# Optimization experiments

Hardware: AMD Instinct MI355X
Metric: run time of the kernel (lower is better)

## Reference

```python
import jax, jax.numpy as jnp
import numpy as np

BN_EPS = 1e-5


def setup_inputs() -> dict:
    key = jax.random.key(0)
    ks = jax.random.split(key, 10)
    N, E, D = 100000, 1600000, 64
    node_feats = jax.random.normal(ks[0], (N, D), dtype=jnp.float32)
    edge_feats = jax.random.randint(ks[1], (E, 3), 0, 2, dtype=jnp.int64)
    edge_index = jax.random.randint(ks[2], (2, E), 0, N, dtype=jnp.int64)
    return {
        "node_feats": node_feats,
        "edge_feats": edge_feats,
        "edge_index": edge_index,
        "num_nodes": N,
        "num_edges": E,
        "eps": jnp.zeros((1,), jnp.float32),
        "bond_emb0": jax.random.normal(ks[3], (5, D), dtype=jnp.float32) * 0.05,
        "bond_emb1": jax.random.normal(ks[4], (6, D), dtype=jnp.float32) * 0.05,
        "bond_emb2": jax.random.normal(ks[5], (2, D), dtype=jnp.float32) * 0.05,
        "W1": jax.random.normal(ks[6], (2 * D, D), dtype=jnp.float32) * (1.0 / np.sqrt(D)),
        "b1": jnp.zeros((2 * D,), jnp.float32),
        "gamma": jnp.ones((2 * D,), jnp.float32),
        "beta": jnp.zeros((2 * D,), jnp.float32),
        "W2": jax.random.normal(ks[7], (D, 2 * D), dtype=jnp.float32) * (1.0 / np.sqrt(2 * D)),
        "b2": jnp.zeros((D,), jnp.float32),
    }


def reference(node_feats, edge_feats, edge_index, num_nodes, num_edges,
              eps, bond_emb0, bond_emb1, bond_emb2,
              W1, b1, gamma, beta, W2, b2):
    # BondEncoder: sum of categorical embeddings over 3 bond features -> [E, D]
    edge_emb = (bond_emb0[edge_feats[:, 0]]
                + bond_emb1[edge_feats[:, 1]]
                + bond_emb2[edge_feats[:, 2]])
    # gather source-node feats (edge_index[1]), combine, relu -> [E, D]
    message = jax.nn.relu(node_feats[edge_index[1]] + edge_emb)
    # scatter_add into target nodes (edge_index[0]) -> [N, D]
    message_reduce = jax.ops.segment_sum(message, edge_index[0], num_segments=num_nodes)
    h = (1.0 + eps) * node_feats + message_reduce  # eps shape [1] broadcasts
    # MLP: Linear -> BatchNorm1d (training-mode batch stats) -> ReLU -> Linear
    h1 = h @ W1.T + b1  # [N, 2D]
    mean = jnp.mean(h1, axis=0)
    var = jnp.mean(jnp.square(h1 - mean), axis=0)  # biased variance (torch BN)
    h1 = gamma * (h1 - mean) * jax.lax.rsqrt(var + BN_EPS) + beta
    h1 = jax.nn.relu(h1)
    return h1 @ W2.T + b2  # [N, D]
```

## Files before the change

### kernel.cpp

```cpp
#include <hip/hip_runtime.h>
#include <stdint.h>

#define D    64
#define D2   128
#define R    98
#define NBK  1024
#define CAP  2176
#define NTRI 2144

__global__ void k_embsum(
    const float* __restrict__ be0, const float* __restrict__ be1,
    const float* __restrict__ be2, float* __restrict__ embsum,
    int* __restrict__ bcursor)
{
    int c = blockIdx.x;
    int t = threadIdx.x;
    if (c < 60) {
        int f0 = c / 12;
        int r  = c % 12;
        int f1 = r / 2;
        int f2 = r % 2;
        embsum[c * D + t] = be0[f0 * D + t] + be1[f1 * D + t] + be2[f2 * D + t];
    } else {
        int i = (c - 60) * 64 + t;
        if (i < NBK) bcursor[i * 16] = i * CAP;
    }
}

__global__ __launch_bounds__(512) void k_part(
    const int* __restrict__ ei, const int* __restrict__ ef,
    int* __restrict__ bcursor, int* __restrict__ payload, int E)
{
    __shared__ int scnt[NBK];
    __shared__ int sstart[NBK];
    __shared__ int sgbase[NBK];
    __shared__ int sdat[4096];
    __shared__ unsigned short sbkt[4096];
    __shared__ int sred2[512];

    int t = threadIdx.x;
    for (int i = t; i < NBK; i += 512) scnt[i] = 0;
    __syncthreads();

    int base2 = blockIdx.x * 2048;

    int b0[4], p0[4], r0[4];
    int b1[4], p1[4], r1[4];

    #pragma unroll
    for (int k = 0; k < 4; k++) {
        int i2 = base2 + k * 512 + t;
        int e0 = i2 * 2;
        if (e0 < E) {
            int2 d  = ((const int2*)ei)[i2];
            int2 s  = ((const int2*)(ei + E))[i2];
            int2 q0 = ((const int2*)ef)[3 * i2 + 0];
            int2 q1 = ((const int2*)ef)[3 * i2 + 1];
            int2 q2 = ((const int2*)ef)[3 * i2 + 2];
            {
                int bb = d.x / R; if (bb > NBK - 1) bb = NBK - 1;
                int ld = d.x - bb * R;
                int code = q0.x * 12 + q0.y * 2 + q1.x;
                b0[k] = bb;
                p0[k] = s.x | (code << 17) | (ld << 23);
                r0[k] = atomicAdd(&scnt[bb], 1);
            }
            if (e0 + 1 < E) {
                int bb = d.y / R; if (bb > NBK - 1) bb = NBK - 1;
                int ld = d.y - bb * R;
                int code = q1.y * 12 + q2.x * 2 + q2.y;
                b1[k] = bb;
                p1[k] = s.y | (code << 17) | (ld << 23);
                r1[k] = atomicAdd(&scnt[bb], 1);
            }
        }
    }
    __syncthreads();

    int c0 = scnt[t * 2], c1 = scnt[t * 2 + 1];
    sred2[t] = c0 + c1;
    __syncthreads();
    int sv = sred2[t];
    for (int off = 1; off < 512; off <<= 1) {
        int x = (t >= off) ? sred2[t - off] : 0;
        __syncthreads();
        sred2[t] += x;
        __syncthreads();
    }
    int excl = sred2[t] - sv;
    sstart[t * 2]     = excl;
    sstart[t * 2 + 1] = excl + c0;
    __syncthreads();

    for (int i = t; i < NBK; i += 512) {
        int c = scnt[i];
        if (c) sgbase[i] = atomicAdd(&bcursor[i * 16], c);
    }
    __syncthreads();

    #pragma unroll
    for (int k = 0; k < 4; k++) {
        int i2 = base2 + k * 512 + t;
        int e0 = i2 * 2;
        if (e0 < E) {
            int slot = sstart[b0[k]] + r0[k];
            sdat[slot] = p0[k]; sbkt[slot] = (unsigned short)b0[k];
            if (e0 + 1 < E) {
                slot = sstart[b1[k]] + r1[k];
                sdat[slot] = p1[k]; sbkt[slot] = (unsigned short)b1[k];
            }
        }
    }
    __syncthreads();

    int tc = E - base2 * 2; if (tc > 4096) tc = 4096;
    #pragma unroll
    for (int k = 0; k < 8; k++) {
        int i = k * 512 + t;
        if (i < tc) {
            int bb = sbkt[i];
            int pos = sgbase[bb] + (i - sstart[bb]);
            if (pos < (bb + 1) * CAP) payload[pos] = sdat[i];
        }
    }
}

__global__ __launch_bounds__(512, 8) void k_sortred(
    const float* __restrict__ nf,
    const int* __restrict__ bcursor,
    int* __restrict__ payload,
    const float* __restrict__ embsum,
    const float* __restrict__ epsp,
    float* __restrict__ h, int N)
{
    __shared__ float sE[60 * D];
    __shared__ int   sq[CAP];
    __shared__ int   scn[R + 1];
    __shared__ int   scur[R];
    __shared__ int   sscan[128];

    int tid = threadIdx.x;
    int b = blockIdx.x;
    int n0 = b * R;

    for (int i = tid; i < 60 * D; i += 512) sE[i] = embsum[i];
    if (tid <= R) scn[tid] = 0;
    __syncthreads();

    int js = b * CAP;
    int cnt = bcursor[b * 16] - js;
    if (cnt > CAP) cnt = CAP;
    if (cnt < 0) cnt = 0;

    for (int i = tid; i < cnt; i += 512)
        atomicAdd(&scn[((unsigned)payload[js + i] >> 23) + 1], 1);
    __syncthreads();

    if (tid < 128) sscan[tid] = (tid <= R) ? scn[tid] : 0;
    __syncthreads();
    for (int off = 1; off < 128; off <<= 1) {
        int x = 0;
        if (tid < 128 && tid >= off) x = sscan[tid - off];
        __syncthreads();
        if (tid < 128) sscan[tid] += x;
        __syncthreads();
    }
    if (tid <= R) {
        scn[tid] = sscan[tid];
        if (tid < R) scur[tid] = sscan[tid];
    }
    __syncthreads();

    for (int i = tid; i < cnt; i += 512) {
        int u = payload[js + i];
        int pos = atomicAdd(&scur[(unsigned)u >> 23], 1);
        sq[pos] = u;
    }
    __syncthreads();

    int w = tid >> 6, l = tid & 63;
    float epsv = 1.0f + epsp[0];
    for (int r = w; r < R; r += 8) {
        int n = n0 + r;
        if (n >= N) break;
        int st = scn[r], en = scn[r + 1];
        float acc = 0.0f;
        for (int jb = st; jb < en; jb += 64) {
            int u = (jb + l < en) ? sq[jb + l] : 0;
            int m = en - jb; if (m > 64) m = 64;
            int t = 0;
            for (; t + 4 <= m; t += 4) {
                int a0 = __shfl(u, t + 0);
                int a1 = __shfl(u, t + 1);
                int a2 = __shfl(u, t + 2);
                int a3 = __shfl(u, t + 3);
                float x0 = nf[(size_t)(a0 & 0x1FFFF) * D + l];
                float x1 = nf[(size_t)(a1 & 0x1FFFF) * D + l];
                float x2 = nf[(size_t)(a2 & 0x1FFFF) * D + l];
                float x3 = nf[(size_t)(a3 & 0x1FFFF) * D + l];
                float e0 = sE[((a0 >> 17) & 63) * D + l];
                float e1 = sE[((a1 >> 17) & 63) * D + l];
                float e2 = sE[((a2 >> 17) & 63) * D + l];
                float e3 = sE[((a3 >> 17) & 63) * D + l];
                acc += fmaxf(x0 + e0, 0.0f) + fmaxf(x1 + e1, 0.0f)
                     + fmaxf(x2 + e2, 0.0f) + fmaxf(x3 + e3, 0.0f);
            }
            for (; t < m; t++) {
                int a = __shfl(u, t);
                acc += fmaxf(nf[(size_t)(a & 0x1FFFF) * D + l]
                             + sE[((a >> 17) & 63) * D + l], 0.0f);
            }
        }
        h[(size_t)n * D + l] = fmaf(epsv, nf[(size_t)n * D + l], acc);
    }
    __syncthreads();

    float* P = (float*)(payload + (size_t)b * CAP);
    const float4* h4 = (const float4*)h;
    if (tid < 256) {
        int iB = tid >> 4, jB = tid & 15;
        float M[4][4];
        #pragma unroll
        for (int a = 0; a < 4; a++)
            #pragma unroll
            for (int c = 0; c < 4; c++) M[a][c] = 0.0f;
        #pragma unroll 2
        for (int n2 = 0; n2 < R; n2++) {
            int n = n0 + n2;
            if (n >= N) break;
            float4 a = h4[(size_t)n * 16 + iB];
            float4 c = h4[(size_t)n * 16 + jB];
            M[0][0] = fmaf(a.x, c.x, M[0][0]);
            M[0][1] = fmaf(a.x, c.y, M[0][1]);
            M[0][2] = fmaf(a.x, c.z, M[0][2]);
            M[0][3] = fmaf(a.x, c.w, M[0][3]);
            M[1][0] = fmaf(a.y, c.x, M[1][0]);
            M[1][1] = fmaf(a.y, c.y, M[1][1]);
            M[1][2] = fmaf(a.y, c.z, M[1][2]);
            M[1][3] = fmaf(a.y, c.w, M[1][3]);
            M[2][0] = fmaf(a.z, c.x, M[2][0]);
            M[2][1] = fmaf(a.z, c.y, M[2][1]);
            M[2][2] = fmaf(a.z, c.z, M[2][2]);
            M[2][3] = fmaf(a.z, c.w, M[2][3]);
            M[3][0] = fmaf(a.w, c.x, M[3][0]);
            M[3][1] = fmaf(a.w, c.y, M[3][1]);
            M[3][2] = fmaf(a.w, c.z, M[3][2]);
            M[3][3] = fmaf(a.w, c.w, M[3][3]);
        }
        #pragma unroll
        for (int a = 0; a < 4; a++)
            #pragma unroll
            for (int c = 0; c < 4; c++) {
                int gi = iB * 4 + a, gj = jB * 4 + c;
                if (gi <= gj)
                    P[gi * 64 + gj - ((gi * (gi + 1)) >> 1)] = M[a][c];
            }
    } else if (tid < 320) {
        int lc = tid - 256;
        float s = 0.0f;
        for (int n2 = 0; n2 < R; n2++) {
            int n = n0 + n2;
            if (n >= N) break;
            s += h[(size_t)n * D + lc];
        }
        P[2080 + lc] = s;
    }
}

__global__ __launch_bounds__(512) void k_redM(
    const float* __restrict__ pM, int nblk,
    float* __restrict__ Mbar, float invN)
{
    __shared__ float sred[512];
    int tid = threadIdx.x;
    int eq = tid & 63, bq = tid >> 6;
    int e = blockIdx.x * 64 + eq;

    int src;
    if (e < 4096) {
        int i = e >> 6, j = e & 63;
        int a = i < j ? i : j;
        int b2 = i < j ? j : i;
        src = a * 64 + b2 - ((a * (a + 1)) >> 1);
    } else {
        src = 2080 + (e - 4096);
    }

    float s0 = 0.0f, s1 = 0.0f, s2 = 0.0f, s3 = 0.0f;
    int b = bq;
    for (; b + 24 < nblk; b += 32) {
        s0 += pM[(size_t)(b +  0) * CAP + src];
        s1 += pM[(size_t)(b +  8) * CAP + src];
        s2 += pM[(size_t)(b + 16) * CAP + src];
        s3 += pM[(size_t)(b + 24) * CAP + src];
    }
    for (; b < nblk; b += 8) s0 += pM[(size_t)b * CAP + src];
    sred[tid] = (s0 + s1) + (s2 + s3);
    __syncthreads();
    if (tid < 64) {
        float s = 0.0f;
        #pragma unroll
        for (int q = 0; q < 8; q++) s += sred[q * 64 + tid];
        Mbar[e] = s * invN;
    }
}

__global__ __launch_bounds__(64) void k_bn(
    const float* __restrict__ Mbar,
    const float* __restrict__ W1,
    const float* __restrict__ b1,
    const float* __restrict__ gamma, const float* __restrict__ beta,
    float* __restrict__ ss)
{
    int c = blockIdx.x;
    int k = threadIdx.x;

    float wk = W1[c * D + k];
    float dk = wk * Mbar[4096 + k];

    float tk = 0.0f;
    #pragma unroll 8
    for (int j = 0; j < 64; j++)
        tk = fmaf(Mbar[k * 64 + j], W1[c * D + j], tk);
    float qk = wk * tk;

    #pragma unroll
    for (int off = 32; off > 0; off >>= 1) {
        dk += __shfl_xor(dk, off);
        qk += __shfl_xor(qk, off);
    }

    if (k == 0) {
        float var  = fmaxf(qk - dk * dk, 0.0f);
        float mean = dk + b1[c];
        float sc   = gamma[c] * rsqrtf(var + 1e-5f);
        ss[c]       = sc;
        ss[128 + c] = beta[c] - mean * sc;
    }
}

#define ABS 132
__global__ __launch_bounds__(512) void k_gemm2(
    const float* __restrict__ h,
    const float* __restrict__ W1,
    const float* __restrict__ b1,
    const float* __restrict__ ss,
    const float* __restrict__ W2,
    const float* __restrict__ b2v,
    float* __restrict__ out,
    int N, int tiles)
{
    __shared__ float AB[128 * ABS];
    __shared__ float W1t[64 * 128];
    __shared__ float W2t[128 * 64];

    int tid = threadIdx.x;

    {
        int c  = tid >> 2;
        int k0 = (tid & 3) * 16;
        const float4* wr = (const float4*)(W1 + c * D + k0);
        #pragma unroll
        for (int q = 0; q < 4; q++) {
            float4 u = wr[q];
            int k = k0 + q * 4;
            W1t[(k + 0) * 128 + c] = u.x;
            W1t[(k + 1) * 128 + c] = u.y;
            W1t[(k + 2) * 128 + c] = u.z;
            W1t[(k + 3) * 128 + c] = u.w;
        }
    }
    {
        int j  = tid >> 3;
        int k0 = (tid & 7) * 16;
        const float4* wr = (const float4*)(W2 + j * D2 + k0);
        #pragma unroll
        for (int q = 0; q < 4; q++) {
            float4 u = wr[q];
            int k = k0 + q * 4;
            W2t[(k + 0) * 64 + j] = u.x;
            W2t[(k + 1) * 64 + j] = u.y;
            W2t[(k + 2) * 64 + j] = u.z;
            W2t[(k + 3) * 64 + j] = u.w;
        }
    }

    int rg = tid >> 5, cg = tid & 31;
    float bb0 = b1[cg * 4 + 0];
    float bb1 = b1[cg * 4 + 1];
    float bb2 = b1[cg * 4 + 2];
    float bb3 = b1[cg * 4 + 3];
    float4 scv = *(const float4*)&ss[cg * 4];
    float4 shv = *(const float4*)&ss[128 + cg * 4];

    int r2 = tid >> 4, c2 = tid & 15;
    float4 obv = *(const float4*)&b2v[c2 * 4];

    int sr = tid >> 2;
    int sc16 = (tid & 3) * 16;

    float4 pf[4];
    #pragma unroll
    for (int q = 0; q < 4; q++) pf[q] = make_float4(0.f, 0.f, 0.f, 0.f);
    {
        int gr = blockIdx.x * 128 + sr;
        if (gr < N) {
            const float4* hrow = (const float4*)(h + (size_t)gr * D + sc16);
            #pragma unroll
            for (int q = 0; q < 4; q++) pf[q] = hrow[q];
        }
    }

    for (int t = blockIdx.x; t < tiles; t += gridDim.x) {
        int row0 = t * 128;
        __syncthreads();
        {
            float* dstp = &AB[sr * ABS + sc16];
            #pragma unroll
            for (int q = 0; q < 4; q++) ((float4*)dstp)[q] = pf[q];
        }
        __syncthreads();

        float acc[8][4];
        #pragma unroll
        for (int i = 0; i < 8; i++)
            #pragma unroll
            for (int j = 0; j < 4; j++) acc[i][j] = 0.0f;

        #pragma unroll 2
        for (int k4 = 0; k4 < 16; k4++) {
            float4 w0 = *(const float4*)&W1t[(k4 * 4 + 0) * 128 + cg * 4];
            float4 w1 = *(const float4*)&W1t[(k4 * 4 + 1) * 128 + cg * 4];
            float4 w2 = *(const float4*)&W1t[(k4 * 4 + 2) * 128 + cg * 4];
            float4 w3 = *(const float4*)&W1t[(k4 * 4 + 3) * 128 + cg * 4];
            #pragma unroll
            for (int i = 0; i < 8; i++) {
                float4 a = *(const float4*)&AB[(rg * 8 + i) * ABS + k4 * 4];
                acc[i][0] = fmaf(a.x, w0.x, acc[i][0]);
                acc[i][1] = fmaf(a.x, w0.y, acc[i][1]);
                acc[i][2] = fmaf(a.x, w0.z, acc[i][2]);
                acc[i][3] = fmaf(a.x, w0.w, acc[i][3]);
                acc[i][0] = fmaf(a.y, w1.x, acc[i][0]);
                acc[i][1] = fmaf(a.y, w1.y, acc[i][1]);
                acc[i][2] = fmaf(a.y, w1.z, acc[i][2]);
                acc[i][3] = fmaf(a.y, w1.w, acc[i][3]);
                acc[i][0] = fmaf(a.z, w2.x, acc[i][0]);
                acc[i][1] = fmaf(a.z, w2.y, acc[i][1]);
                acc[i][2] = fmaf(a.z, w2.z, acc[i][2]);
                acc[i][3] = fmaf(a.z, w2.w, acc[i][3]);
                acc[i][0] = fmaf(a.w, w3.x, acc[i][0]);
                acc[i][1] = fmaf(a.w, w3.y, acc[i][1]);
                acc[i][2] = fmaf(a.w, w3.z, acc[i][2]);
                acc[i][3] = fmaf(a.w, w3.w, acc[i][3]);
            }
        }
        __syncthreads();

        int tn = t + gridDim.x;
        #pragma unroll
        for (int q = 0; q < 4; q++) pf[q] = make_float4(0.f, 0.f, 0.f, 0.f);
        if (tn < tiles) {
            int gr = tn * 128 + sr;
            if (gr < N) {
                const float4* hrow = (const float4*)(h + (size_t)gr * D + sc16);
                #pragma unroll
                for (int q = 0; q < 4; q++) pf[q] = hrow[q];
            }
        }

        #pragma unroll
        for (int i = 0; i < 8; i++) {
            float g0 = fmaxf(fmaf(acc[i][0] + bb0, scv.x, shv.x), 0.0f);
            float g1 = fmaxf(fmaf(acc[i][1] + bb1, scv.y, shv.y), 0.0f);
            float g2 = fmaxf(fmaf(acc[i][2] + bb2, scv.z, shv.z), 0.0f);
            float g3 = fmaxf(fmaf(acc[i][3] + bb3, scv.w, shv.w), 0.0f);
            *(float4*)&AB[(rg * 8 + i) * ABS + cg * 4] = make_float4(g0, g1, g2, g3);
        }
        __syncthreads();

        float acc2[4][4];
        #pragma unroll
        for (int i = 0; i < 4; i++)
            #pragma unroll
            for (int j = 0; j < 4; j++) acc2[i][j] = 0.0f;

        #pragma unroll 2
        for (int k4 = 0; k4 < 32; k4++) {
            float4 u0 = *(const float4*)&W2t[(k4 * 4 + 0) * 64 + c2 * 4];
            float4 u1 = *(const float4*)&W2t[(k4 * 4 + 1) * 64 + c2 * 4];
            float4 u2 = *(const float4*)&W2t[(k4 * 4 + 2) * 64 + c2 * 4];
            float4 u3 = *(const float4*)&W2t[(k4 * 4 + 3) * 64 + c2 * 4];
            #pragma unroll
            for (int i = 0; i < 4; i++) {
                float4 g = *(const float4*)&AB[(r2 * 4 + i) * ABS + k4 * 4];
                acc2[i][0] = fmaf(g.x, u0.x, acc2[i][0]);
                acc2[i][1] = fmaf(g.x, u0.y, acc2[i][1]);
                acc2[i][2] = fmaf(g.x, u0.z, acc2[i][2]);
                acc2[i][3] = fmaf(g.x, u0.w, acc2[i][3]);
                acc2[i][0] = fmaf(g.y, u1.x, acc2[i][0]);
                acc2[i][1] = fmaf(g.y, u1.y, acc2[i][1]);
                acc2[i][2] = fmaf(g.y, u1.z, acc2[i][2]);
                acc2[i][3] = fmaf(g.y, u1.w, acc2[i][3]);
                acc2[i][0] = fmaf(g.z, u2.x, acc2[i][0]);
                acc2[i][1] = fmaf(g.z, u2.y, acc2[i][1]);
                acc2[i][2] = fmaf(g.z, u2.z, acc2[i][2]);
                acc2[i][3] = fmaf(g.z, u2.w, acc2[i][3]);
                acc2[i][0] = fmaf(g.w, u3.x, acc2[i][0]);
                acc2[i][1] = fmaf(g.w, u3.y, acc2[i][1]);
                acc2[i][2] = fmaf(g.w, u3.z, acc2[i][2]);
                acc2[i][3] = fmaf(g.w, u3.w, acc2[i][3]);
            }
        }

        #pragma unroll
        for (int i = 0; i < 4; i++) {
            int gr = row0 + r2 * 4 + i;
            if (gr < N) {
                float4 pk = make_float4(acc2[i][0] + obv.x, acc2[i][1] + obv.y,
                                        acc2[i][2] + obv.z, acc2[i][3] + obv.w);
                *(float4*)&out[(size_t)gr * D + c2 * 4] = pk;
            }
        }
    }
}

extern "C" void kernel_launch(void* const* d_in, const int* in_sizes, int n_in,
                              void* d_out, int out_size, void* d_ws, size_t ws_size,
                              hipStream_t stream)
{
    const float* nf    = (const float*)d_in[0];
    const int*   ef    = (const int*)d_in[1];
    const int*   ei    = (const int*)d_in[2];
    const float* epsp  = (const float*)d_in[5];
    const float* be0   = (const float*)d_in[6];
    const float* be1   = (const float*)d_in[7];
    const float* be2   = (const float*)d_in[8];
    const float* W1    = (const float*)d_in[9];
    const float* b1    = (const float*)d_in[10];
    const float* gamma = (const float*)d_in[11];
    const float* beta  = (const float*)d_in[12];
    const float* W2    = (const float*)d_in[13];
    const float* b2v   = (const float*)d_in[14];
    float*       out   = (float*)d_out;

    int N = in_sizes[0] / D;
    int E = in_sizes[1] / 3;

    int tiles2 = (N + 127) / 128;
    int g2 = 256;

    float* h       = (float*)d_ws;
    float* Mbar    = h + (size_t)N * D;
    float* ss      = Mbar + 4224;
    float* embsum  = ss + 256;
    int*   bcursor = (int*)(embsum + 60 * D);
    int*   payload = bcursor + NBK * 16;
    float* pM      = (float*)payload;

    k_embsum<<<76, 64, 0, stream>>>(be0, be1, be2, embsum, bcursor);

    int E2 = (E + 1) / 2;
    int gP = (E2 + 2047) / 2048;
    k_part<<<gP, 512, 0, stream>>>(ei, ef, bcursor, payload, E);

    k_sortred<<<NBK, 512, 0, stream>>>(nf, bcursor, payload, embsum, epsp, h, N);

    k_redM<<<65, 512, 0, stream>>>(pM, NBK, Mbar, 1.0f / (float)N);
    k_bn<<<128, 64, 0, stream>>>(Mbar, W1, b1, gamma, beta, ss);

    k_gemm2<<<g2, 512, 0, stream>>>(h, W1, b1, ss, W2, b2v, out, N, tiles2);
}
```

Baseline: 351.3 us.

## Split sortred and gemm2 launches in halves and parallelize Mbar reduction with atomics

Splits k_sortred and k_gemm2 each into two half-size launches on the same stream. It also widens k_redM from 65 to 260 blocks, each summing a quarter of the partial blocks and combining results with atomicAdd into Mbar, which k_embsum now zeroes. The wider reduction targets poor occupancy in k_redM. The launch splitting adds launch overhead and gives no overlap on a single stream. The atomic accumulation also makes summation order nondeterministic.

```diff
diff --git a/kernel.cpp b/kernel.cpp
--- a/kernel.cpp
+++ b/kernel.cpp
@@ -11,7 +11,7 @@
 __global__ void k_embsum(
     const float* __restrict__ be0, const float* __restrict__ be1,
     const float* __restrict__ be2, float* __restrict__ embsum,
-    int* __restrict__ bcursor)
+    int* __restrict__ bcursor, float* __restrict__ Mbar)
 {
     int c = blockIdx.x;
     int t = threadIdx.x;
@@ -21,9 +21,12 @@
         int f1 = r / 2;
         int f2 = r % 2;
         embsum[c * D + t] = be0[f0 * D + t] + be1[f1 * D + t] + be2[f2 * D + t];
-    } else {
+    } else if (c < 76) {
         int i = (c - 60) * 64 + t;
         if (i < NBK) bcursor[i * 16] = i * CAP;
+    } else {
+        int i = (c - 76) * 64 + t;
+        Mbar[i] = 0.0f;
     }
 }
 
@@ -131,7 +134,7 @@
     int* __restrict__ payload,
     const float* __restrict__ embsum,
     const float* __restrict__ epsp,
-    float* __restrict__ h, int N)
+    float* __restrict__ h, int N, int b0)
 {
     __shared__ float sE[60 * D];
     __shared__ int   sq[CAP];
@@ -140,7 +143,7 @@
     __shared__ int   sscan[128];
 
     int tid = threadIdx.x;
-    int b = blockIdx.x;
+    int b = b0 + blockIdx.x;
     int n0 = b * R;
 
     for (int i = tid; i < 60 * D; i += 512) sE[i] = embsum[i];
@@ -268,13 +271,15 @@
 }
 
 __global__ __launch_bounds__(512) void k_redM(
-    const float* __restrict__ pM, int nblk,
+    const float* __restrict__ pM,
     float* __restrict__ Mbar, float invN)
 {
     __shared__ float sred[512];
     int tid = threadIdx.x;
     int eq = tid & 63, bq = tid >> 6;
-    int e = blockIdx.x * 64 + eq;
+    int ec = blockIdx.x >> 2;
+    int qg = blockIdx.x & 3;
+    int e  = ec * 64 + eq;
 
     int src;
     if (e < 4096) {
@@ -286,22 +291,21 @@
         src = 2080 + (e - 4096);
     }
 
+    int bbase = qg * 256;
     float s0 = 0.0f, s1 = 0.0f, s2 = 0.0f, s3 = 0.0f;
-    int b = bq;
-    for (; b + 24 < nblk; b += 32) {
-        s0 += pM[(size_t)(b +  0) * CAP + src];
-        s1 += pM[(size_t)(b +  8) * CAP + src];
-        s2 += pM[(size_t)(b + 16) * CAP + src];
-        s3 += pM[(size_t)(b + 24) * CAP + src];
-    }
-    for (; b < nblk; b += 8) s0 += pM[(size_t)b * CAP + src];
+    for (int b = bq; b < 256; b += 32) {
+        s0 += pM[(size_t)(bbase + b +  0) * CAP + src];
+        s1 += pM[(size_t)(bbase + b +  8) * CAP + src];
+        s2 += pM[(size_t)(bbase + b + 16) * CAP + src];
+        s3 += pM[(size_t)(bbase + b + 24) * CAP + src];
+    }
     sred[tid] = (s0 + s1) + (s2 + s3);
     __syncthreads();
     if (tid < 64) {
         float s = 0.0f;
         #pragma unroll
         for (int q = 0; q < 8; q++) s += sred[q * 64 + tid];
-        Mbar[e] = s * invN;
+        atomicAdd(&Mbar[e], s * invN);
     }
 }
 
@@ -348,7 +352,7 @@
     const float* __restrict__ W2,
     const float* __restrict__ b2v,
     float* __restrict__ out,
-    int N, int tiles)
+    int N, int tBeg, int tEnd)
 {
     __shared__ float AB[128 * ABS];
     __shared__ float W1t[64 * 128];
@@ -403,7 +407,7 @@
     #pragma unroll
     for (int q = 0; q < 4; q++) pf[q] = make_float4(0.f, 0.f, 0.f, 0.f);
     {
-        int gr = blockIdx.x * 128 + sr;
+        int gr = (tBeg + blockIdx.x) * 128 + sr;
         if (gr < N) {
             const float4* hrow = (const float4*)(h + (size_t)gr * D + sc16);
             #pragma unroll
@@ -411,7 +415,7 @@
         }
     }
 
-    for (int t = blockIdx.x; t < tiles; t += gridDim.x) {
+    for (int t = tBeg + blockIdx.x; t < tEnd; t += gridDim.x) {
         int row0 = t * 128;
         __syncthreads();
         {
@@ -459,7 +463,7 @@
         int tn = t + gridDim.x;
         #pragma unroll
         for (int q = 0; q < 4; q++) pf[q] = make_float4(0.f, 0.f, 0.f, 0.f);
-        if (tn < tiles) {
+        if (tn < tEnd) {
             int gr = tn * 128 + sr;
             if (gr < N) {
                 const float4* hrow = (const float4*)(h + (size_t)gr * D + sc16);
@@ -547,7 +551,7 @@
     int E = in_sizes[1] / 3;
 
     int tiles2 = (N + 127) / 128;
-    int g2 = 256;
+    int tMid   = (tiles2 + 1) / 2;
 
     float* h       = (float*)d_ws;
     float* Mbar    = h + (size_t)N * D;
@@ -557,16 +561,18 @@
     int*   payload = bcursor + NBK * 16;
     float* pM      = (float*)payload;
 
-    k_embsum<<<76, 64, 0, stream>>>(be0, be1, be2, embsum, bcursor);
+    k_embsum<<<142, 64, 0, stream>>>(be0, be1, be2, embsum, bcursor, Mbar);
 
     int E2 = (E + 1) / 2;
     int gP = (E2 + 2047) / 2048;
     k_part<<<gP, 512, 0, stream>>>(ei, ef, bcursor, payload, E);
 
-    k_sortred<<<NBK, 512, 0, stream>>>(nf, bcursor, payload, embsum, epsp, h, N);
-
-    k_redM<<<65, 512, 0, stream>>>(pM, NBK, Mbar, 1.0f / (float)N);
+    k_sortred<<<NBK / 2, 512, 0, stream>>>(nf, bcursor, payload, embsum, epsp, h, N, 0);
+    k_sortred<<<NBK / 2, 512, 0, stream>>>(nf, bcursor, payload, embsum, epsp, h, N, NBK / 2);
+
+    k_redM<<<260, 512, 0, stream>>>(pM, Mbar, 1.0f / (float)N);
     k_bn<<<128, 64, 0, stream>>>(Mbar, W1, b1, gamma, beta, ss);
 
-    k_gemm2<<<g2, 512, 0, stream>>>(h, W1, b1, ss, W2, b2v, out, N, tiles2);
-}
+    k_gemm2<<<256, 512, 0, stream>>>(h, W1, b1, ss, W2, b2v, out, N, 0, tMid);
+    k_gemm2<<<256, 512, 0, stream>>>(h, W1, b1, ss, W2, b2v, out, N, tMid, tiles2);
+}
```

Result: slower. 367.7 us (+4.6%).
